# Optimization experiments

Measured on AMD Instinct MI355X. Metric: run time of the kernel, lower is better.

## Reference

```python
import jax, jax.numpy as jnp
import numpy as np

C = 343.0      # speed of sound (init kwarg c)
F = 16         # number of frequency channels (len(omega))
H = 128        # MLP hidden width
N = 131072     # collocation points


def _mlp(coords, W1, b1, W2, b2, W3, b3):
    # coords: [..., 3] -> [..., 2F] (first F = real part, last F = imag part)
    h = jnp.tanh(coords @ W1 + b1)
    h = jnp.tanh(h @ W2 + b2)
    return h @ W3 + b3


def setup_inputs() -> dict:
    key = jax.random.key(0)
    ks = jax.random.split(key, 4)
    inputs = jax.random.normal(ks[0], (N, 3), dtype=jnp.float32)
    # omega = 2*pi*f for f = 100..1600 Hz (matches init kwarg list)
    omega = 2.0 * jnp.pi * 100.0 * jnp.arange(1, F + 1, dtype=jnp.float32)
    s_in = 1.0 / np.sqrt(3.0)
    s_h = 1.0 / np.sqrt(float(H))
    W1 = jax.random.normal(ks[1], (3, H), dtype=jnp.float32) * s_in
    b1 = jnp.zeros((H,), dtype=jnp.float32)
    W2 = jax.random.normal(ks[2], (H, H), dtype=jnp.float32) * s_h
    b2 = jnp.zeros((H,), dtype=jnp.float32)
    W3 = jax.random.normal(ks[3], (H, 2 * F), dtype=jnp.float32) * s_h
    b3 = jnp.zeros((2 * F,), dtype=jnp.float32)
    return {"inputs": inputs, "omega": omega, "W1": W1, "b1": b1,
            "W2": W2, "b2": b2, "W3": W3, "b3": b3}


def reference(inputs, omega, W1, b1, W2, b2, W3, b3):
    # Pointwise network R^3 -> R^{2F} (real/imag stacked).
    f = lambda c3: _mlp(c3, W1, b1, W2, b2, W3, b3)

    # u: complex pressure per point per frequency, [N, F]
    out = _mlp(inputs, W1, b1, W2, b2, W3, b3)           # [N, 2F]
    u = out[:, :F] + 1j * out[:, F:]

    # Full spatial Hessian per point via forward-over-reverse AD (fused
    # replacement for the torch per-channel autograd.grad loop).
    hess = jax.vmap(jax.jacfwd(jax.jacrev(f)))(inputs)   # [N, 2F, 3, 3]
    lap_ri = jnp.einsum('nfii->nf', hess)                # diagonal trace = Laplacian
    lap = lap_ri[:, :F] + 1j * lap_ri[:, F:]             # [N, F] complex

    # PDE residual skips channel 0, exactly as the torch loop (i+1 indexing).
    k2 = (omega[1:] / C) ** 2                            # [F-1]
    residual = lap[:, 1:] + k2 * u[:, 1:]                # [N, F-1]

    # mean over channels then over batch == global mean of |residual|^2
    return jnp.mean(jnp.abs(residual) ** 2)
```

## Files before the change

kernel.cpp:

```cpp
#include <hip/hip_runtime.h>
#include <math.h>

#ifndef __has_builtin
#define __has_builtin(x) 0
#endif

#define NPTS   131072
#define FCH    16
#define CSND   343.0f
#define PB     16
#define BLOCK  256
#define GRID   768
#define NBLK   (NPTS / PB)

typedef _Float16 half8 __attribute__((ext_vector_type(8)));
typedef _Float16 half2v __attribute__((ext_vector_type(2)));
typedef float    f32x4 __attribute__((ext_vector_type(4)));

static __device__ __forceinline__ unsigned pack2(float a, float b) {
#if __has_builtin(__builtin_amdgcn_cvt_pkrtz)
  return __builtin_bit_cast(unsigned, __builtin_amdgcn_cvt_pkrtz(a, b));
#else
  half2v v; v[0] = (_Float16)a; v[1] = (_Float16)b;
  return __builtin_bit_cast(unsigned, v);
#endif
}

static __device__ __forceinline__ float mytanh(float x) {
#if __has_builtin(__builtin_amdgcn_exp2f)
  float e = __builtin_amdgcn_exp2f(2.885390082f * x);
#else
  float e = __expf(2.0f * x);
#endif
  return fmaf(-2.0f, __builtin_amdgcn_rcpf(e + 1.0f), 1.0f);
}


__global__ __launch_bounds__(BLOCK, 3) void helmholtz_kernel(
    const float* __restrict__ x,
    const float* __restrict__ omega,
    const float* __restrict__ W1,
    const float* __restrict__ b1,
    const float* __restrict__ W2,
    const float* __restrict__ b2,
    const float* __restrict__ W3,
    const float* __restrict__ b3,
    float* __restrict__ out)
{
  __shared__ unsigned s_A[80 * 64];
  __shared__ unsigned s_HG[16 * 128];

  const int tid  = threadIdx.x;
  const int w    = tid >> 6;
  const int l    = tid & 63;
  const int col  = l & 15;
  const int quad = l >> 4;
  const int nh   = w & 1;

  const int pA = tid >> 4;
  const int g  = tid & 15;
  float wx[8], wy[8], wz[8], bB[8];
#pragma unroll
  for (int u = 0; u < 8; u++) {
    int unit = 8 * g + u;
    wx[u] = W1[unit]; wy[u] = W1[128 + unit]; wz[u] = W1[256 + unit];
    bB[u] = b1[unit];
  }

  half8 w2f[2][4];
#pragma unroll
  for (int ntl = 0; ntl < 2; ntl++) {
    const int n = 32 * w + 16 * ntl + col;
#pragma unroll
    for (int ks = 0; ks < 4; ks++) {
      half8 f;
#pragma unroll
      for (int j8 = 0; j8 < 8; j8++)
        f[j8] = (_Float16)W2[(ks * 32 + (quad << 3) + j8) * 128 + n];
      w2f[ntl][ks] = f;
    }
  }
  half8 w3f[4];
#pragma unroll
  for (int ks = 0; ks < 4; ks++) {
    half8 f;
#pragma unroll
    for (int j8 = 0; j8 < 8; j8++) {
      int kap = ks * 32 + (quad << 3) + j8;
      int q   = kap >> 1;
      int j   = 32 * (q >> 4) + 16 * (kap & 1) + (q & 15);
      f[j8] = (_Float16)W3[j * 32 + 16 * nh + col];
    }
    w3f[ks] = f;
  }

  const float b2r0 = b2[32 * w + col];
  const float b2r1 = b2[32 * w + 16 + col];
  float k2v = 0.0f;
  if (col >= 1) {
    float om = omega[col] * (1.0f / CSND);
    k2v = om * om;
  }
  const float b3v = b3[16 * nh + col];

  float wsum = 0.0f;
  float xr0, xr1, xr2;

  auto loadX = [&](int blk) {
    const float* xp = x + (size_t)(blk * PB + pA) * 3;
    xr0 = xp[0]; xr1 = xp[1]; xr2 = xp[2];
  };

  auto phaseA = [&]() {
    const int cbase = (g ^ pA) << 2;
    float t[8], s[8];
#pragma unroll
    for (int u = 0; u < 8; u++) {
      float z = fmaf(xr0, wx[u], fmaf(xr1, wy[u], fmaf(xr2, wz[u], bB[u])));
      t[u] = mytanh(z);
      s[u] = 1.0f - t[u] * t[u];
    }
    uint4 q;
    q = make_uint4(pack2(t[0], t[1]), pack2(t[2], t[3]),
                   pack2(t[4], t[5]), pack2(t[6], t[7]));
    *(uint4*)&s_A[(pA)      * 64 + cbase] = q;
    q = make_uint4(pack2(s[0]*wx[0], s[1]*wx[1]), pack2(s[2]*wx[2], s[3]*wx[3]),
                   pack2(s[4]*wx[4], s[5]*wx[5]), pack2(s[6]*wx[6], s[7]*wx[7]));
    *(uint4*)&s_A[(16 + pA) * 64 + cbase] = q;
    q = make_uint4(pack2(s[0]*wy[0], s[1]*wy[1]), pack2(s[2]*wy[2], s[3]*wy[3]),
                   pack2(s[4]*wy[4], s[5]*wy[5]), pack2(s[6]*wy[6], s[7]*wy[7]));
    *(uint4*)&s_A[(32 + pA) * 64 + cbase] = q;
    q = make_uint4(pack2(s[0]*wz[0], s[1]*wz[1]), pack2(s[2]*wz[2], s[3]*wz[3]),
                   pack2(s[4]*wz[4], s[5]*wz[5]), pack2(s[6]*wz[6], s[7]*wz[7]));
    *(uint4*)&s_A[(48 + pA) * 64 + cbase] = q;
    float c[8];
#pragma unroll
    for (int u = 0; u < 8; u++) {
      float wq = fmaf(wx[u], wx[u], fmaf(wy[u], wy[u], wz[u] * wz[u]));
      c[u] = -2.0f * t[u] * s[u] * wq;
    }
    q = make_uint4(pack2(c[0], c[1]), pack2(c[2], c[3]),
                   pack2(c[4], c[5]), pack2(c[6], c[7]));
    *(uint4*)&s_A[(64 + pA) * 64 + cbase] = q;
  };

  auto phaseDE = [&]() {
    const int pbase = col * 128;
    f32x4 dy = (f32x4){0.0f, 0.0f, 0.0f, 0.0f};
    f32x4 dl = (f32x4){0.0f, 0.0f, 0.0f, 0.0f};
#pragma unroll
    for (int ks = 0; ks < 4; ks++) {
      int pos = ((((ks << 2) + quad) ^ col) << 2);
      half8 afy = *(const half8*)&s_HG[pbase + pos];
      half8 afl = *(const half8*)&s_HG[pbase + 64 + pos];
      dy = __builtin_amdgcn_mfma_f32_16x16x32_f16(afy, w3f[ks], dy, 0, 0, 0);
      dl = __builtin_amdgcn_mfma_f32_16x16x32_f16(afl, w3f[ks], dl, 0, 0, 0);
    }
    if (col >= 1) {
#pragma unroll
      for (int r = 0; r < 4; r++) {
        float yv  = dy[r] + b3v;
        float res = fmaf(k2v, yv, dl[r]);
        wsum += res * res;
      }
    }
  };

  loadX(blockIdx.x);
  bool first = true;
  for (int blk = blockIdx.x; blk < NBLK; blk += gridDim.x) {
    if (!first && w < 2) phaseDE();
    first = false;
    phaseA();
    __syncthreads();

    int nblk = blk + (int)gridDim.x;
    if (nblk < NBLK) loadX(nblk);

    f32x4 acc[5][2];
#pragma unroll
    for (int v = 0; v < 5; v++)
#pragma unroll
      for (int ntl = 0; ntl < 2; ntl++)
        acc[v][ntl] = (f32x4){0.0f, 0.0f, 0.0f, 0.0f};

#pragma unroll
    for (int v = 0; v < 5; v++) {
      const int rb = (v * 16 + col) * 64;
#pragma unroll
      for (int ks = 0; ks < 4; ks++) {
        half8 af = *(const half8*)&s_A[rb + ((((ks << 2) + quad) ^ col) << 2)];
        acc[v][0] = __builtin_amdgcn_mfma_f32_16x16x32_f16(af, w2f[0][ks], acc[v][0], 0, 0, 0);
        acc[v][1] = __builtin_amdgcn_mfma_f32_16x16x32_f16(af, w2f[1][ks], acc[v][1], 0, 0, 0);
      }
    }

#pragma unroll
    for (int r = 0; r < 4; r++) {
      int p = (quad << 2) + r;
      float t2[2], gg[2];
#pragma unroll
      for (int ntl = 0; ntl < 2; ntl++) {
        float z2 = acc[0][ntl][r] + (ntl ? b2r1 : b2r0);
        float d0 = acc[1][ntl][r], d1 = acc[2][ntl][r], d2 = acc[3][ntl][r];
        float Av = acc[4][ntl][r];
        float t  = mytanh(z2);
        float s2 = 1.0f - t * t;
        t2[ntl] = t;
        gg[ntl] = s2 * (Av - 2.0f * t * (d0 * d0 + d1 * d1 + d2 * d2));
      }
      int q   = 16 * w + col;
      int pos = (((q >> 2) ^ p) << 2) + (q & 3);
      s_HG[p * 128 + pos]      = pack2(t2[0], t2[1]);
      s_HG[p * 128 + 64 + pos] = pack2(gg[0], gg[1]);
    }
    __syncthreads();
  }
  if (w < 2) phaseDE();

#pragma unroll
  for (int off = 32; off > 0; off >>= 1)
    wsum += __shfl_down(wsum, off, 64);
  if (l == 0)
    atomicAdd(out, wsum * (1.0f / ((float)NPTS * (float)(FCH - 1))));
}

extern "C" void kernel_launch(void* const* d_in, const int* in_sizes, int n_in,
                              void* d_out, int out_size, void* d_ws, size_t ws_size,
                              hipStream_t stream) {
  const float* x     = (const float*)d_in[0];
  const float* omega = (const float*)d_in[1];
  const float* W1    = (const float*)d_in[2];
  const float* b1    = (const float*)d_in[3];
  const float* W2    = (const float*)d_in[4];
  const float* b2    = (const float*)d_in[5];
  const float* W3    = (const float*)d_in[6];
  const float* b3    = (const float*)d_in[7];
  float* out = (float*)d_out;

  (void)hipMemsetAsync(out, 0, sizeof(float), stream);
  helmholtz_kernel<<<GRID, BLOCK, 0, stream>>>(x, omega, W1, b1, W2, b2, W3, b3, out);
}
```

Measured before the change: 128.7 us.

## Double-buffer LDS stages and compute elementwise math in packed fp16

Shared-memory tiles for the first-layer features and the hidden/gradient stage become double-buffered, so each iteration computes layer 1 for the next block while running the layer-2 MFMAs on the current one, leaving one barrier per iteration. The elementwise derivative math in both phases moves to packed half2 arithmetic to halve VALU work. Grid size and launch-bounds occupancy drop to fit the doubled LDS. The fp16 elementwise math lowers precision of pre-activations and curvature terms, which may hurt accuracy.

```diff
diff --git a/kernel.cpp b/kernel.cpp
--- a/kernel.cpp
+++ b/kernel.cpp
@@ -10,20 +10,23 @@
 #define CSND   343.0f
 #define PB     16
 #define BLOCK  256
-#define GRID   768
+#define GRID   512
 #define NBLK   (NPTS / PB)
 
 typedef _Float16 half8 __attribute__((ext_vector_type(8)));
-typedef _Float16 half2v __attribute__((ext_vector_type(2)));
+typedef _Float16 h2 __attribute__((ext_vector_type(2)));
 typedef float    f32x4 __attribute__((ext_vector_type(4)));
 
-static __device__ __forceinline__ unsigned pack2(float a, float b) {
+static __device__ __forceinline__ h2 ph2(float a, float b) {
 #if __has_builtin(__builtin_amdgcn_cvt_pkrtz)
-  return __builtin_bit_cast(unsigned, __builtin_amdgcn_cvt_pkrtz(a, b));
+  return __builtin_bit_cast(h2, __builtin_amdgcn_cvt_pkrtz(a, b));
 #else
-  half2v v; v[0] = (_Float16)a; v[1] = (_Float16)b;
+  h2 v; v[0] = (_Float16)a; v[1] = (_Float16)b;
+  return v;
+#endif
+}
+static __device__ __forceinline__ unsigned bc(h2 v) {
   return __builtin_bit_cast(unsigned, v);
-#endif
 }
 
 static __device__ __forceinline__ float mytanh(float x) {
@@ -36,7 +39,7 @@
 }
 
 
-__global__ __launch_bounds__(BLOCK, 3) void helmholtz_kernel(
+__global__ __launch_bounds__(BLOCK, 2) void helmholtz_kernel(
     const float* __restrict__ x,
     const float* __restrict__ omega,
     const float* __restrict__ W1,
@@ -47,8 +50,8 @@
     const float* __restrict__ b3,
     float* __restrict__ out)
 {
-  __shared__ unsigned s_A[80 * 64];
-  __shared__ unsigned s_HG[16 * 128];
+  __shared__ unsigned s_A[2][80 * 64];
+  __shared__ unsigned s_HG[2][16 * 128];
 
   const int tid  = threadIdx.x;
   const int w    = tid >> 6;
@@ -59,12 +62,16 @@
 
   const int pA = tid >> 4;
   const int g  = tid & 15;
-  float wx[8], wy[8], wz[8], bB[8];
-#pragma unroll
-  for (int u = 0; u < 8; u++) {
-    int unit = 8 * g + u;
-    wx[u] = W1[unit]; wy[u] = W1[128 + unit]; wz[u] = W1[256 + unit];
-    bB[u] = b1[unit];
+  h2 wx2[4], wy2[4], wz2[4], bB2[4], m2wq2[4];
+#pragma unroll
+  for (int u2 = 0; u2 < 4; u2++) {
+    int u0 = 8 * g + 2 * u2, u1 = u0 + 1;
+    float ax = W1[u0], ay = W1[128 + u0], az = W1[256 + u0];
+    float bx = W1[u1], by = W1[128 + u1], bz = W1[256 + u1];
+    wx2[u2] = ph2(ax, bx); wy2[u2] = ph2(ay, by); wz2[u2] = ph2(az, bz);
+    bB2[u2] = ph2(b1[u0], b1[u1]);
+    m2wq2[u2] = ph2(-2.0f * (ax * ax + ay * ay + az * az),
+                    -2.0f * (bx * bx + by * by + bz * bz));
   }
 
   half8 w2f[2][4];
@@ -102,57 +109,50 @@
     k2v = om * om;
   }
   const float b3v = b3[16 * nh + col];
+  const h2 one2 = {(_Float16)1.0f, (_Float16)1.0f};
+  const h2 m2c  = {(_Float16)-2.0f, (_Float16)-2.0f};
 
   float wsum = 0.0f;
-  float xr0, xr1, xr2;
-
-  auto loadX = [&](int blk) {
+
+  auto phaseA = [&](int blk, int buf) {
     const float* xp = x + (size_t)(blk * PB + pA) * 3;
-    xr0 = xp[0]; xr1 = xp[1]; xr2 = xp[2];
+    float x0 = xp[0], x1 = xp[1], x2 = xp[2];
+    h2 xh0 = ph2(x0, x0), xh1 = ph2(x1, x1), xh2 = ph2(x2, x2);
+    h2 tp[4], sp[4];
+#pragma unroll
+    for (int u2 = 0; u2 < 4; u2++) {
+      h2 z = xh0 * wx2[u2] + xh1 * wy2[u2] + xh2 * wz2[u2] + bB2[u2];
+      float t0 = mytanh((float)z[0]);
+      float t1 = mytanh((float)z[1]);
+      tp[u2] = ph2(t0, t1);
+      sp[u2] = one2 - tp[u2] * tp[u2];
+    }
+    unsigned* sA = s_A[buf];
+    const int cbase = (g ^ pA) << 2;
+    uint4 q;
+    q = make_uint4(bc(tp[0]), bc(tp[1]), bc(tp[2]), bc(tp[3]));
+    *(uint4*)&sA[(pA)      * 64 + cbase] = q;
+    q = make_uint4(bc(sp[0]*wx2[0]), bc(sp[1]*wx2[1]), bc(sp[2]*wx2[2]), bc(sp[3]*wx2[3]));
+    *(uint4*)&sA[(16 + pA) * 64 + cbase] = q;
+    q = make_uint4(bc(sp[0]*wy2[0]), bc(sp[1]*wy2[1]), bc(sp[2]*wy2[2]), bc(sp[3]*wy2[3]));
+    *(uint4*)&sA[(32 + pA) * 64 + cbase] = q;
+    q = make_uint4(bc(sp[0]*wz2[0]), bc(sp[1]*wz2[1]), bc(sp[2]*wz2[2]), bc(sp[3]*wz2[3]));
+    *(uint4*)&sA[(48 + pA) * 64 + cbase] = q;
+    q = make_uint4(bc((tp[0]*sp[0])*m2wq2[0]), bc((tp[1]*sp[1])*m2wq2[1]),
+                   bc((tp[2]*sp[2])*m2wq2[2]), bc((tp[3]*sp[3])*m2wq2[3]));
+    *(uint4*)&sA[(64 + pA) * 64 + cbase] = q;
   };
 
-  auto phaseA = [&]() {
-    const int cbase = (g ^ pA) << 2;
-    float t[8], s[8];
-#pragma unroll
-    for (int u = 0; u < 8; u++) {
-      float z = fmaf(xr0, wx[u], fmaf(xr1, wy[u], fmaf(xr2, wz[u], bB[u])));
-      t[u] = mytanh(z);
-      s[u] = 1.0f - t[u] * t[u];
-    }
-    uint4 q;
-    q = make_uint4(pack2(t[0], t[1]), pack2(t[2], t[3]),
-                   pack2(t[4], t[5]), pack2(t[6], t[7]));
-    *(uint4*)&s_A[(pA)      * 64 + cbase] = q;
-    q = make_uint4(pack2(s[0]*wx[0], s[1]*wx[1]), pack2(s[2]*wx[2], s[3]*wx[3]),
-                   pack2(s[4]*wx[4], s[5]*wx[5]), pack2(s[6]*wx[6], s[7]*wx[7]));
-    *(uint4*)&s_A[(16 + pA) * 64 + cbase] = q;
-    q = make_uint4(pack2(s[0]*wy[0], s[1]*wy[1]), pack2(s[2]*wy[2], s[3]*wy[3]),
-                   pack2(s[4]*wy[4], s[5]*wy[5]), pack2(s[6]*wy[6], s[7]*wy[7]));
-    *(uint4*)&s_A[(32 + pA) * 64 + cbase] = q;
-    q = make_uint4(pack2(s[0]*wz[0], s[1]*wz[1]), pack2(s[2]*wz[2], s[3]*wz[3]),
-                   pack2(s[4]*wz[4], s[5]*wz[5]), pack2(s[6]*wz[6], s[7]*wz[7]));
-    *(uint4*)&s_A[(48 + pA) * 64 + cbase] = q;
-    float c[8];
-#pragma unroll
-    for (int u = 0; u < 8; u++) {
-      float wq = fmaf(wx[u], wx[u], fmaf(wy[u], wy[u], wz[u] * wz[u]));
-      c[u] = -2.0f * t[u] * s[u] * wq;
-    }
-    q = make_uint4(pack2(c[0], c[1]), pack2(c[2], c[3]),
-                   pack2(c[4], c[5]), pack2(c[6], c[7]));
-    *(uint4*)&s_A[(64 + pA) * 64 + cbase] = q;
-  };
-
-  auto phaseDE = [&]() {
+  auto phaseDE = [&](int buf) {
+    const unsigned* hgb = s_HG[buf];
     const int pbase = col * 128;
     f32x4 dy = (f32x4){0.0f, 0.0f, 0.0f, 0.0f};
     f32x4 dl = (f32x4){0.0f, 0.0f, 0.0f, 0.0f};
 #pragma unroll
     for (int ks = 0; ks < 4; ks++) {
       int pos = ((((ks << 2) + quad) ^ col) << 2);
-      half8 afy = *(const half8*)&s_HG[pbase + pos];
-      half8 afl = *(const half8*)&s_HG[pbase + 64 + pos];
+      half8 afy = *(const half8*)&hgb[pbase + pos];
+      half8 afl = *(const half8*)&hgb[pbase + 64 + pos];
       dy = __builtin_amdgcn_mfma_f32_16x16x32_f16(afy, w3f[ks], dy, 0, 0, 0);
       dl = __builtin_amdgcn_mfma_f32_16x16x32_f16(afl, w3f[ks], dl, 0, 0, 0);
     }
@@ -166,17 +166,17 @@
     }
   };
 
-  loadX(blockIdx.x);
-  bool first = true;
-  for (int blk = blockIdx.x; blk < NBLK; blk += gridDim.x) {
-    if (!first && w < 2) phaseDE();
-    first = false;
-    phaseA();
-    __syncthreads();
+  phaseA(blockIdx.x, 0);
+  __syncthreads();
+
+  int parity = 0;
+  for (int blk = blockIdx.x; blk < NBLK; blk += gridDim.x, parity ^= 1) {
+    if (w < 2 && blk != (int)blockIdx.x) phaseDE(parity ^ 1);
 
     int nblk = blk + (int)gridDim.x;
-    if (nblk < NBLK) loadX(nblk);
-
+    if (nblk < NBLK) phaseA(nblk, parity ^ 1);
+
+    const unsigned* sA = s_A[parity];
     f32x4 acc[5][2];
 #pragma unroll
     for (int v = 0; v < 5; v++)
@@ -189,34 +189,37 @@
       const int rb = (v * 16 + col) * 64;
 #pragma unroll
       for (int ks = 0; ks < 4; ks++) {
-        half8 af = *(const half8*)&s_A[rb + ((((ks << 2) + quad) ^ col) << 2)];
+        half8 af = *(const half8*)&sA[rb + ((((ks << 2) + quad) ^ col) << 2)];
         acc[v][0] = __builtin_amdgcn_mfma_f32_16x16x32_f16(af, w2f[0][ks], acc[v][0], 0, 0, 0);
         acc[v][1] = __builtin_amdgcn_mfma_f32_16x16x32_f16(af, w2f[1][ks], acc[v][1], 0, 0, 0);
       }
     }
 
-#pragma unroll
-    for (int r = 0; r < 4; r++) {
-      int p = (quad << 2) + r;
-      float t2[2], gg[2];
-#pragma unroll
-      for (int ntl = 0; ntl < 2; ntl++) {
-        float z2 = acc[0][ntl][r] + (ntl ? b2r1 : b2r0);
-        float d0 = acc[1][ntl][r], d1 = acc[2][ntl][r], d2 = acc[3][ntl][r];
-        float Av = acc[4][ntl][r];
-        float t  = mytanh(z2);
-        float s2 = 1.0f - t * t;
-        t2[ntl] = t;
-        gg[ntl] = s2 * (Av - 2.0f * t * (d0 * d0 + d1 * d1 + d2 * d2));
+    {
+      unsigned* hg = s_HG[parity];
+#pragma unroll
+      for (int r = 0; r < 4; r++) {
+        int p = (quad << 2) + r;
+        float t0 = mytanh(acc[0][0][r] + b2r0);
+        float t1 = mytanh(acc[0][1][r] + b2r1);
+        h2 tp = ph2(t0, t1);
+        h2 sp = one2 - tp * tp;
+        h2 d0 = ph2(acc[1][0][r], acc[1][1][r]);
+        h2 d1 = ph2(acc[2][0][r], acc[2][1][r]);
+        h2 d2 = ph2(acc[3][0][r], acc[3][1][r]);
+        h2 Ap = ph2(acc[4][0][r], acc[4][1][r]);
+        h2 Bp = d0 * d0 + d1 * d1 + d2 * d2;
+        h2 gg = sp * (Ap + m2c * (tp * Bp));
+        int q   = 16 * w + col;
+        int pos = (((q >> 2) ^ p) << 2) + (q & 3);
+        hg[p * 128 + pos]      = bc(tp);
+        hg[p * 128 + 64 + pos] = bc(gg);
       }
-      int q   = 16 * w + col;
-      int pos = (((q >> 2) ^ p) << 2) + (q & 3);
-      s_HG[p * 128 + pos]      = pack2(t2[0], t2[1]);
-      s_HG[p * 128 + 64 + pos] = pack2(gg[0], gg[1]);
     }
     __syncthreads();
   }
-  if (w < 2) phaseDE();
+
+  if (w < 2) phaseDE(parity ^ 1);
 
 #pragma unroll
   for (int off = 32; off > 0; off >>= 1)
```

Measured after the change: 121.1 us, median of 2. 5.9% less time.
